# Performance work log

Hardware: AMD Instinct MI355X
Metric: run time of the kernel (lower is better)

Reference implementation:

```python
import jax, jax.numpy as jnp
import numpy as np

B, N, D = 8, 512, 512          # batch, seq_len, n_units (== d_in for residual)
H = 8                          # n_heads
DH = D // H                    # head dim
POS_CLIP = 60
EPS = 1e-7


def setup_inputs() -> dict:
    key = jax.random.key(0)
    ks = jax.random.split(key, 16)
    s = 0.02
    inp = {
        "query": jax.random.normal(ks[0], (B, N, D), dtype=jnp.float32),
        "valid_len": jax.random.randint(ks[1], (B,), 256, N + 1, dtype=jnp.int32),
        "Wq": jax.random.normal(ks[2], (D, D), dtype=jnp.float32) * s,
        "bq": jnp.zeros((D,), jnp.float32),
        "Wk": jax.random.normal(ks[3], (D, D), dtype=jnp.float32) * s,
        "bk": jnp.zeros((D,), jnp.float32),
        "Wv": jax.random.normal(ks[4], (D, D), dtype=jnp.float32) * s,
        "bv": jnp.zeros((D,), jnp.float32),
        "Wh": jax.random.normal(ks[5], (D, D), dtype=jnp.float32) * s,
        "bh": jnp.zeros((D,), jnp.float32),
        "pos_k": jax.random.uniform(ks[6], (2 * POS_CLIP + 1, DH), dtype=jnp.float32, minval=-0.05, maxval=0.05),
        "conv1_w": jax.random.normal(ks[7], (5, 5, H, 2 * H), dtype=jnp.float32) * s,  # HWIO
        "conv1_b": jnp.zeros((2 * H,), jnp.float32),
        "norm1_gamma": jnp.ones((2 * H,), jnp.float32),
        "norm1_beta": jnp.zeros((2 * H,), jnp.float32),
        "conv2_w": jax.random.normal(ks[8], (5, 5, 2 * H, H), dtype=jnp.float32) * s,
        "conv2_b": jnp.zeros((H,), jnp.float32),
        "ln_gamma": jnp.ones((D,), jnp.float32),
        "ln_beta": jnp.zeros((D,), jnp.float32),
    }
    return inp


def _conv_same(x, k, b):
    # x: [b, n, n, cin], k: [kh, kw, cin, cout] -> [b, n, n, cout]
    y = jax.lax.conv_general_dilated(x, k, window_strides=(1, 1), padding="SAME",
                                     dimension_numbers=("NHWC", "HWIO", "NHWC"))
    return y + b


def _norm_masked(x, valid_len, gamma, beta):
    # Norm(axes=[1,2]) with tf.nn.weighted_moments; mask over the query axis (axis 1).
    b, n, m, c = x.shape
    w = (jnp.arange(n)[None, :] < valid_len[:, None]).astype(x.dtype)  # [b, n]
    w4 = w[:, :, None, None]
    sw = valid_len.astype(x.dtype)[:, None, None, None] * m            # sum of broadcast weights
    mean = jnp.sum(w4 * x, axis=(1, 2), keepdims=True) / sw
    var = jnp.sum(w4 * (x - mean) ** 2, axis=(1, 2), keepdims=True) / sw
    return gamma * (x - mean) * jax.lax.rsqrt(var + EPS) + beta


def reference(query, valid_len, Wq, bq, Wk, bk, Wv, bv, Wh, bh, pos_k,
              conv1_w, conv1_b, norm1_gamma, norm1_beta, conv2_w, conv2_b,
              ln_gamma, ln_beta):
    b, n, d_in = query.shape
    # relative position indices (Shaw et al.), clipped to +/- POS_CLIP
    rel = jnp.clip(jnp.arange(n)[None, :] - jnp.arange(n)[:, None], -POS_CLIP, POS_CLIP) + POS_CLIP
    pos_enc = pos_k[rel]                                   # [n, n, dh]

    def heads(x):
        # tf.concat(tf.split(x, H, -1), 0): head-major blocks of size b
        return x.reshape(b, n, H, DH).transpose(2, 0, 1, 3)  # [h, b, n, dh]

    q = heads(query @ Wq + bq)
    k = heads(query @ Wk + bk)
    v = heads(query @ Wv + bv)

    scores = jnp.einsum("hbnd,hbmd->hbnm", q, k) + jnp.einsum("hbnd,nmd->hbnm", q, pos_enc)
    scores = scores / jnp.sqrt(jnp.asarray(DH, scores.dtype))

    # SelfCNN over attention maps: [b, n, n, h]
    maps = scores.transpose(1, 2, 3, 0)
    y = _conv_same(maps, conv1_w, conv1_b)
    y = _norm_masked(y, valid_len, norm1_gamma, norm1_beta)
    y = jax.nn.relu(y)
    y = _conv_same(y, conv2_w, conv2_b)                    # [b, n, n, h]
    scores = y.transpose(3, 0, 1, 2)                       # [h, b, n, m]

    seq_mask = jnp.arange(n)[None, :] < valid_len[:, None]  # [b, n] over key axis
    scores = jnp.where(seq_mask[None, :, None, :], scores, jnp.asarray(-1e12, scores.dtype))
    attn = jax.nn.softmax(scores, axis=-1)

    out = jnp.einsum("hbnm,hbmd->hbnd", attn, v)
    out = out.transpose(1, 2, 0, 3).reshape(b, n, H * DH)  # merge heads back
    out = out @ Wh + bh + query                            # residual

    mean = jnp.mean(out, axis=-1, keepdims=True)
    var = jnp.var(out, axis=-1, keepdims=True)
    return ln_gamma * (out - mean) * jax.lax.rsqrt(var + EPS) + ln_beta
```

## Files before the change

kernel.cpp:

```cpp
#include <hip/hip_runtime.h>

#define PC_ 60

typedef unsigned short u16;
typedef __attribute__((ext_vector_type(8))) short short8v;
typedef __attribute__((ext_vector_type(4))) float f32x4;

__device__ inline float bf2f(u16 u) {
    union { unsigned int i; float f; } x; x.i = ((unsigned)u) << 16; return x.f;
}
__device__ inline u16 f2bf(float f) {
    union { float f; unsigned int i; } x; x.f = f;
    unsigned int r = x.i + 0x7fff + ((x.i >> 16) & 1);
    return (u16)(r >> 16);
}
__device__ inline unsigned pk2(float a, float b) {
    return (unsigned)f2bf(a) | ((unsigned)f2bf(b) << 16);
}

__global__ __launch_bounds__(256) void k_prepx(const float* __restrict__ X, u16* __restrict__ Xb)
{
    const int i = (blockIdx.x * 256 + threadIdx.x) * 8;
    float4 a = *reinterpret_cast<const float4*>(X + i);
    float4 b = *reinterpret_cast<const float4*>(X + i + 4);
    *reinterpret_cast<uint4*>(Xb + i) =
        make_uint4(pk2(a.x, a.y), pk2(a.z, a.w), pk2(b.x, b.y), pk2(b.z, b.w));
}

__global__ __launch_bounds__(256) void k_prept(
    const float* __restrict__ W0, const float* __restrict__ W1,
    const float* __restrict__ W2, const float* __restrict__ W3,
    u16* __restrict__ T0, u16* __restrict__ T1, u16* __restrict__ T2, u16* __restrict__ T3)
{
    const int z = blockIdx.z;
    const float* W = (z == 0) ? W0 : (z == 1) ? W1 : (z == 2) ? W2 : W3;
    u16* T        = (z == 0) ? T0 : (z == 1) ? T1 : (z == 2) ? T2 : T3;
    __shared__ float ls[64 * 65];
    const int k0 = blockIdx.x * 64, n0 = blockIdx.y * 64;
    const int t = threadIdx.x;
#pragma unroll
    for (int i = 0; i < 16; ++i) {
        const int idx = t + i * 256, r = idx >> 6, c = idx & 63;
        ls[c * 65 + r] = W[(size_t)(k0 + r) * 512 + n0 + c];
    }
    __syncthreads();
#pragma unroll
    for (int i = 0; i < 16; ++i) {
        const int idx = t + i * 256, r = idx >> 6, c = idx & 63;
        T[(size_t)(n0 + r) * 512 + k0 + c] = f2bf(ls[r * 65 + c]);
    }
}

__global__ void k_wprep(const float* __restrict__ c1w, const float* __restrict__ c2w,
                        const float* __restrict__ pos_k,
                        u16* __restrict__ Wf1, u16* __restrict__ Wf2, u16* __restrict__ pos_kb)
{
    const int t = threadIdx.x;
    for (int s = t; s < 448; s += 256) {
        const int q = s >> 6, l = s & 63, lg = l >> 4, n = l & 15;
        const int G = q * 4 + lg;
        unsigned o[4];
#pragma unroll
        for (int u2 = 0; u2 < 4; ++u2) {
            float v0 = 0.f, v1 = 0.f;
            if (G < 25) {
                const int dn = G / 5, dm = G - dn * 5;
                v0 = c1w[((dn * 5 + dm) * 8 + u2 * 2 + 0) * 16 + n];
                v1 = c1w[((dn * 5 + dm) * 8 + u2 * 2 + 1) * 16 + n];
            }
            o[u2] = pk2(v0, v1);
        }
        *reinterpret_cast<uint4*>(&Wf1[s * 8]) = make_uint4(o[0], o[1], o[2], o[3]);
    }
    for (int s = t; s < 832; s += 256) {
        const int q = s >> 6, l = s & 63, lg = l >> 4, n = l & 15;
        const int G = q * 4 + lg;
        unsigned o[4];
#pragma unroll
        for (int u2 = 0; u2 < 4; ++u2) {
            float v0 = 0.f, v1 = 0.f;
            if (G < 50 && n < 8) {
                const int pos = G >> 1, h = G & 1;
                const int dn = pos / 5, dm = pos - dn * 5;
                v0 = c2w[((dn * 5 + dm) * 16 + h * 8 + u2 * 2 + 0) * 8 + n];
                v1 = c2w[((dn * 5 + dm) * 16 + h * 8 + u2 * 2 + 1) * 8 + n];
            }
            o[u2] = pk2(v0, v1);
        }
        *reinterpret_cast<uint4*>(&Wf2[s * 8]) = make_uint4(o[0], o[1], o[2], o[3]);
    }
    for (int s = t; s < 128 * 64; s += 256) {
        const int r = s >> 6;
        pos_kb[s] = (r < 121) ? f2bf(pos_k[s]) : (u16)0;
    }
}

__global__ __launch_bounds__(256) void k_qkvm(
    const u16* __restrict__ Xb,
    const u16* __restrict__ WT0, const u16* __restrict__ WT1, const u16* __restrict__ WT2,
    const float* __restrict__ b0, const float* __restrict__ b1, const float* __restrict__ b2,
    u16* __restrict__ Qb, u16* __restrict__ Kb, u16* __restrict__ Vt)
{
    const int z = blockIdx.z;
    const u16* WT    = (z == 0) ? WT0 : (z == 1) ? WT1 : WT2;
    const float* bias = (z == 0) ? b0 : (z == 1) ? b1 : b2;
    __shared__ __align__(16) u16 sh[18432];
    u16* As = sh; u16* Bs = sh + 9216;
    const int t = threadIdx.x, lane = t & 63, wave = t >> 6;
    const int wm = wave >> 1, wn = wave & 1;
    const int lg = lane >> 4, ln16 = lane & 15;
    const int m0 = blockIdx.x * 128, n0 = blockIdx.y * 128;
    f32x4 acc[4][4] = {};
    for (int k0 = 0; k0 < 512; k0 += 64) {
#pragma unroll
        for (int u = 0; u < 4; ++u) {
            const int chunk = u * 256 + t, row = chunk >> 3, ko = (chunk & 7) * 8;
            *reinterpret_cast<uint4*>(As + row * 72 + ko) =
                *reinterpret_cast<const uint4*>(Xb + (size_t)(m0 + row) * 512 + k0 + ko);
            *reinterpret_cast<uint4*>(Bs + row * 72 + ko) =
                *reinterpret_cast<const uint4*>(WT + (size_t)(n0 + row) * 512 + k0 + ko);
        }
        __syncthreads();
#pragma unroll
        for (int kk = 0; kk < 64; kk += 32) {
            short8v a[4], bfr[4];
#pragma unroll
            for (int mi = 0; mi < 4; ++mi)
                a[mi] = *reinterpret_cast<const short8v*>(As + (wm * 64 + mi * 16 + ln16) * 72 + kk + lg * 8);
#pragma unroll
            for (int ni = 0; ni < 4; ++ni)
                bfr[ni] = *reinterpret_cast<const short8v*>(Bs + (wn * 64 + ni * 16 + ln16) * 72 + kk + lg * 8);
#pragma unroll
            for (int mi = 0; mi < 4; ++mi)
#pragma unroll
                for (int ni = 0; ni < 4; ++ni)
                    acc[mi][ni] = __builtin_amdgcn_mfma_f32_16x16x32_bf16(a[mi], bfr[ni], acc[mi][ni], 0, 0, 0);
        }
        __syncthreads();
    }
    u16* Cs = sh + wave * 4608;
#pragma unroll
    for (int ni = 0; ni < 4; ++ni) {
        const float bv = bias[n0 + wn * 64 + ni * 16 + ln16];
#pragma unroll
        for (int mi = 0; mi < 4; ++mi)
#pragma unroll
            for (int r = 0; r < 4; ++r)
                Cs[(mi * 16 + lg * 4 + r) * 72 + ni * 16 + ln16] = f2bf(acc[mi][ni][r] + bv);
    }
    if (z < 2) {
        u16* O = (z == 0) ? Qb : Kb;
#pragma unroll
        for (int j = 0; j < 8; ++j) {
            const int chunk = j * 64 + lane, row = chunk >> 3, co = (chunk & 7) * 8;
            const int tok = m0 + wm * 64 + row;
            const int b = tok >> 9, n = tok & 511;
            const int cg = n0 + wn * 64 + co;
            const int h = cg >> 6, dh = cg & 63;
            *reinterpret_cast<uint4*>(O + ((size_t)((b * 8 + h) * 512 + n)) * 64 + dh) =
                *reinterpret_cast<const uint4*>(Cs + row * 72 + co);
        }
    } else {
#pragma unroll
        for (int j = 0; j < 8; ++j) {
            const int chunk = j * 64 + lane, dr = chunk >> 3, no8 = (chunk & 7) * 8;
            const int cg = n0 + wn * 64 + dr;
            const int h = cg >> 6, dh = cg & 63;
            const int tok = m0 + wm * 64 + no8;
            const int b = tok >> 9, n = tok & 511;
            u16 v[8];
#pragma unroll
            for (int e = 0; e < 8; ++e) v[e] = Cs[(no8 + e) * 72 + dr];
            uint4 o = make_uint4((unsigned)v[0] | ((unsigned)v[1] << 16),
                                 (unsigned)v[2] | ((unsigned)v[3] << 16),
                                 (unsigned)v[4] | ((unsigned)v[5] << 16),
                                 (unsigned)v[6] | ((unsigned)v[7] << 16));
            *reinterpret_cast<uint4*>(Vt + ((size_t)((b * 8 + h) * 64 + dh)) * 512 + n) = o;
        }
    }
}

__global__ __launch_bounds__(256) void k_qposm(
    const u16* __restrict__ Qb, const u16* __restrict__ pos_kb, u16* __restrict__ QP)
{
    __shared__ __align__(16) u16 sh[18432];
    u16* As = sh; u16* Bs = sh + 9216;
    const int t = threadIdx.x, lane = t & 63, wave = t >> 6;
    const int lg = lane >> 4, ln16 = lane & 15;
    const int n0 = blockIdx.x * 128, bh = blockIdx.y;
#pragma unroll
    for (int u = 0; u < 4; ++u) {
        const int chunk = u * 256 + t, row = chunk >> 3, ko = (chunk & 7) * 8;
        *reinterpret_cast<uint4*>(As + row * 72 + ko) =
            *reinterpret_cast<const uint4*>(Qb + ((size_t)(bh * 512 + n0 + row)) * 64 + ko);
        *reinterpret_cast<uint4*>(Bs + row * 72 + ko) =
            *reinterpret_cast<const uint4*>(pos_kb + (size_t)row * 64 + ko);
    }
    __syncthreads();
    f32x4 acc[2][8] = {};
#pragma unroll
    for (int kk = 0; kk < 64; kk += 32) {
        short8v a[2], bfr[8];
#pragma unroll
        for (int mi = 0; mi < 2; ++mi)
            a[mi] = *reinterpret_cast<const short8v*>(As + (wave * 32 + mi * 16 + ln16) * 72 + kk + lg * 8);
#pragma unroll
        for (int ni = 0; ni < 8; ++ni)
            bfr[ni] = *reinterpret_cast<const short8v*>(Bs + (ni * 16 + ln16) * 72 + kk + lg * 8);
#pragma unroll
        for (int mi = 0; mi < 2; ++mi)
#pragma unroll
            for (int ni = 0; ni < 8; ++ni)
                acc[mi][ni] = __builtin_amdgcn_mfma_f32_16x16x32_bf16(a[mi], bfr[ni], acc[mi][ni], 0, 0, 0);
    }
    __syncthreads();
    u16* Cs = sh + wave * 4352;
#pragma unroll
    for (int mi = 0; mi < 2; ++mi)
#pragma unroll
        for (int ni = 0; ni < 8; ++ni)
#pragma unroll
            for (int r = 0; r < 4; ++r)
                Cs[(mi * 16 + lg * 4 + r) * 136 + ni * 16 + ln16] = f2bf(acc[mi][ni][r]);
#pragma unroll
    for (int j = 0; j < 8; ++j) {
        const int chunk = j * 64 + lane, row = chunk >> 4, co = (chunk & 15) * 8;
        *reinterpret_cast<uint4*>(QP + ((size_t)(bh * 512 + n0 + wave * 32 + row)) * 128 + co) =
            *reinterpret_cast<const uint4*>(Cs + row * 136 + co);
    }
}

__global__ __launch_bounds__(256) void k_scoresm(
    const u16* __restrict__ Qb, const u16* __restrict__ Kb, const u16* __restrict__ QP,
    u16* __restrict__ S)
{
    __shared__ __align__(16) u16 sh[18432];
    u16* As = sh; u16* Bs = sh + 9216;
    const int t = threadIdx.x, lane = t & 63, wave = t >> 6;
    const int wm = wave >> 1, wn = wave & 1;
    const int lg = lane >> 4, ln16 = lane & 15;
    const int m0 = blockIdx.x * 128, n0 = blockIdx.y * 128, bh = blockIdx.z;
#pragma unroll
    for (int u = 0; u < 4; ++u) {
        const int chunk = u * 256 + t, row = chunk >> 3, ko = (chunk & 7) * 8;
        *reinterpret_cast<uint4*>(As + row * 72 + ko) =
            *reinterpret_cast<const uint4*>(Qb + ((size_t)(bh * 512 + n0 + row)) * 64 + ko);
        *reinterpret_cast<uint4*>(Bs + row * 72 + ko) =
            *reinterpret_cast<const uint4*>(Kb + ((size_t)(bh * 512 + m0 + row)) * 64 + ko);
    }
    __syncthreads();
    f32x4 acc[4][4] = {};
#pragma unroll
    for (int kk = 0; kk < 64; kk += 32) {
        short8v a[4], bfr[4];
#pragma unroll
        for (int mi = 0; mi < 4; ++mi)
            a[mi] = *reinterpret_cast<const short8v*>(As + (wm * 64 + mi * 16 + ln16) * 72 + kk + lg * 8);
#pragma unroll
        for (int ni = 0; ni < 4; ++ni)
            bfr[ni] = *reinterpret_cast<const short8v*>(Bs + (wn * 64 + ni * 16 + ln16) * 72 + kk + lg * 8);
#pragma unroll
        for (int mi = 0; mi < 4; ++mi)
#pragma unroll
            for (int ni = 0; ni < 4; ++ni)
                acc[mi][ni] = __builtin_amdgcn_mfma_f32_16x16x32_bf16(a[mi], bfr[ni], acc[mi][ni], 0, 0, 0);
    }
    __syncthreads();
    u16* QPs = sh;
#pragma unroll
    for (int u = 0; u < 8; ++u) {
        const int chunk = u * 256 + t, row = chunk >> 4, co = (chunk & 15) * 8;
        *reinterpret_cast<uint4*>(QPs + row * 128 + co) =
            *reinterpret_cast<const uint4*>(QP + ((size_t)(bh * 512 + n0 + row)) * 128 + co);
    }
    __syncthreads();
#pragma unroll
    for (int mi = 0; mi < 4; ++mi)
#pragma unroll
        for (int ni = 0; ni < 4; ++ni) {
            const int m_g = m0 + wn * 64 + ni * 16 + ln16;
#pragma unroll
            for (int r = 0; r < 4; ++r) {
                const int n_loc = wm * 64 + mi * 16 + lg * 4 + r;
                const int n_g = n0 + n_loc;
                int rel = m_g - n_g;
                rel = rel < -PC_ ? -PC_ : (rel > PC_ ? PC_ : rel);
                const float v = (acc[mi][ni][r] + bf2f(QPs[n_loc * 128 + rel + PC_])) * 0.125f;
                S[(size_t)bh * 262144 + (size_t)n_g * 512 + m_g] = f2bf(v);
            }
        }
}

__global__ __launch_bounds__(256) void k_conv1m(
    const u16* __restrict__ S, const u16* __restrict__ Wf,
    const float* __restrict__ bias, u16* __restrict__ Y,
    const int* __restrict__ VL, float* __restrict__ ST)
{
    __shared__ __align__(16) u16 xs[10368];
    __shared__ float wred[4][16][2];
    const int t = threadIdx.x;
    const int b = blockIdx.z;
    const int n0 = blockIdx.y * 32;
    const int m0 = blockIdx.x * 32;
    const u16* sp0 = S + (size_t)(b * 8) * 262144;
    for (int idx = t; idx < 1296; idx += 256) {
        const int r = idx / 36; const int c = idx - r * 36;
        const int gn = n0 - 2 + r, gm = m0 - 2 + c;
        uint4 pk = make_uint4(0, 0, 0, 0);
        if ((unsigned)gn < 512u && (unsigned)gm < 512u) {
            const u16* p = sp0 + (size_t)gn * 512 + gm;
            u16 v[8];
#pragma unroll
            for (int e = 0; e < 8; ++e) v[e] = p[(size_t)e * 262144];
            pk.x = (unsigned)v[0] | ((unsigned)v[1] << 16);
            pk.y = (unsigned)v[2] | ((unsigned)v[3] << 16);
            pk.z = (unsigned)v[4] | ((unsigned)v[5] << 16);
            pk.w = (unsigned)v[6] | ((unsigned)v[7] << 16);
        }
        *reinterpret_cast<uint4*>(&xs[idx * 8]) = pk;
    }
    const int lane = t & 63, wave = t >> 6;
    const int lg = lane >> 4, ln16 = lane & 15;
    short8v bq[7];
#pragma unroll
    for (int q = 0; q < 7; ++q)
        bq[q] = *reinterpret_cast<const short8v*>(&Wf[(q * 64 + lane) * 8]);
    int aoff[7];
#pragma unroll
    for (int q = 0; q < 7; ++q) {
        const int G = q * 4 + lg; const int p = (G < 25) ? G : 0;
        const int dn = p / 5, dm = p - dn * 5;
        aoff[q] = (dn * 36 + dm) * 8;
    }
    const float bs = bias[ln16];
    const int vl = VL[b];
    float sst = 0.f, sst2 = 0.f;
    __syncthreads();
    for (int i = 0; i < 16; ++i) {
        const int j = wave * 16 + i;
        const int tr = j >> 1, c0 = (j & 1) << 4;
        const int pb = (tr * 36 + c0 + ln16) * 8;
        f32x4 acc = {bs, bs, bs, bs};
#pragma unroll
        for (int q = 0; q < 7; ++q) {
            short8v a = *reinterpret_cast<const short8v*>(&xs[pb + aoff[q]]);
            acc = __builtin_amdgcn_mfma_f32_16x16x32_bf16(a, bq[q], acc, 0, 0, 0);
        }
        u16* yp = Y + (((size_t)(b * 512 + n0 + tr)) * 512 + (m0 + c0 + lg * 4)) * 16 + ln16;
        yp[0]  = f2bf(acc[0]); yp[16] = f2bf(acc[1]);
        yp[32] = f2bf(acc[2]); yp[48] = f2bf(acc[3]);
        if (n0 + tr < vl) {
            sst  += acc[0] + acc[1] + acc[2] + acc[3];
            sst2 += acc[0]*acc[0] + acc[1]*acc[1] + acc[2]*acc[2] + acc[3]*acc[3];
        }
    }
    sst  += __shfl_xor(sst, 16);  sst  += __shfl_xor(sst, 32);
    sst2 += __shfl_xor(sst2, 16); sst2 += __shfl_xor(sst2, 32);
    if (lane < 16) { wred[wave][lane][0] = sst; wred[wave][lane][1] = sst2; }
    __syncthreads();
    if (t < 16) {
        const float a  = wred[0][t][0] + wred[1][t][0] + wred[2][t][0] + wred[3][t][0];
        const float b2 = wred[0][t][1] + wred[1][t][1] + wred[2][t][1] + wred[3][t][1];
        atomicAdd(&ST[(b * 16 + t) * 2 + 0], a);
        atomicAdd(&ST[(b * 16 + t) * 2 + 1], b2);
    }
}

__global__ void k_statfin(const float* __restrict__ ST, const int* __restrict__ VL,
                          const float* __restrict__ g, const float* __restrict__ be,
                          float* __restrict__ ST2)
{
    const int i = threadIdx.x;
    if (i < 128) {
        const int b = i >> 4, c = i & 15;
        const float sw = (float)VL[b] * 512.f;
        const float mean = ST[i * 2] / sw;
        const float var = ST[i * 2 + 1] / sw - mean * mean;
        const float scale = g[c] * rsqrtf(var + 1e-7f);
        ST2[i * 2] = scale;
        ST2[i * 2 + 1] = be[c] - mean * scale;
    }
}

__global__ __launch_bounds__(256) void k_conv2m(
    const u16* __restrict__ Y, const float* __restrict__ ST2,
    const u16* __restrict__ Wf, const float* __restrict__ bias,
    u16* __restrict__ S2)
{
    __shared__ __align__(16) u16 xs[20736];
    const int t = threadIdx.x;
    const int b = blockIdx.z;
    const int n0 = blockIdx.y * 32, m0 = blockIdx.x * 32;
    float sc[16], shv[16];
#pragma unroll
    for (int ch = 0; ch < 16; ++ch) {
        sc[ch]  = ST2[(b * 16 + ch) * 2 + 0];
        shv[ch] = ST2[(b * 16 + ch) * 2 + 1];
    }
    for (int idx = t; idx < 1296; idx += 256) {
        const int r = idx / 36; const int c = idx - r * 36;
        const int gn = n0 - 2 + r, gm = m0 - 2 + c;
        uint4 p0 = make_uint4(0, 0, 0, 0), p1 = p0;
        if ((unsigned)gn < 512u && (unsigned)gm < 512u) {
            const u16* yp = Y + (((size_t)(b * 512 + gn)) * 512 + gm) * 16;
            const uint4 r0 = *reinterpret_cast<const uint4*>(yp);
            const uint4 r1 = *reinterpret_cast<const uint4*>(yp + 8);
            const unsigned w0[4] = {r0.x, r0.y, r0.z, r0.w};
            const unsigned w1[4] = {r1.x, r1.y, r1.z, r1.w};
            unsigned o0[4], o1[4];
#pragma unroll
            for (int u2 = 0; u2 < 4; ++u2) {
                const int ch = u2 * 2;
                float a0 = bf2f((u16)(w0[u2] & 0xffff));
                float a1 = bf2f((u16)(w0[u2] >> 16));
                a0 = fmaf(a0, sc[ch], shv[ch]);          a0 = a0 > 0.f ? a0 : 0.f;
                a1 = fmaf(a1, sc[ch + 1], shv[ch + 1]);  a1 = a1 > 0.f ? a1 : 0.f;
                o0[u2] = pk2(a0, a1);
                const int ch2 = 8 + u2 * 2;
                float b0 = bf2f((u16)(w1[u2] & 0xffff));
                float b1 = bf2f((u16)(w1[u2] >> 16));
                b0 = fmaf(b0, sc[ch2], shv[ch2]);          b0 = b0 > 0.f ? b0 : 0.f;
                b1 = fmaf(b1, sc[ch2 + 1], shv[ch2 + 1]);  b1 = b1 > 0.f ? b1 : 0.f;
                o1[u2] = pk2(b0, b1);
            }
            p0 = make_uint4(o0[0], o0[1], o0[2], o0[3]);
            p1 = make_uint4(o1[0], o1[1], o1[2], o1[3]);
        }
        *reinterpret_cast<uint4*>(&xs[idx * 8]) = p0;
        *reinterpret_cast<uint4*>(&xs[10368 + idx * 8]) = p1;
    }
    const int lane = t & 63, wave = t >> 6;
    const int lg = lane >> 4, ln16 = lane & 15;
    short8v bq[13];
#pragma unroll
    for (int q = 0; q < 13; ++q)
        bq[q] = *reinterpret_cast<const short8v*>(&Wf[(q * 64 + lane) * 8]);
    int aoff[13];
#pragma unroll
    for (int q = 0; q < 13; ++q) {
        const int G = q * 4 + lg; const int p = (G < 50) ? G : 0;
        const int pos = p >> 1, h = p & 1;
        const int dn = pos / 5, dm = pos - dn * 5;
        aoff[q] = h * 10368 + (dn * 36 + dm) * 8;
    }
    const float bs = (ln16 < 8) ? bias[ln16] : 0.f;
    __syncthreads();
    for (int i = 0; i < 16; ++i) {
        const int j = wave * 16 + i;
        const int tr = j >> 1, c0 = (j & 1) << 4;
        const int pb = (tr * 36 + c0 + ln16) * 8;
        f32x4 acc = {bs, bs, bs, bs};
#pragma unroll
        for (int q = 0; q < 13; ++q) {
            short8v a = *reinterpret_cast<const short8v*>(&xs[pb + aoff[q]]);
            acc = __builtin_amdgcn_mfma_f32_16x16x32_bf16(a, bq[q], acc, 0, 0, 0);
        }
        if (ln16 < 8) {
            uint2 o = make_uint2(pk2(acc[0], acc[1]), pk2(acc[2], acc[3]));
            *reinterpret_cast<uint2*>(
                &S2[(((size_t)(b * 8 + ln16)) * 512 + n0 + tr) * 512 + m0 + c0 + lg * 4]) = o;
        }
    }
}

__global__ __launch_bounds__(256) void k_softmax(u16* __restrict__ S,
                                                 const int* __restrict__ VL)
{
    const int row = blockIdx.x * 4 + (threadIdx.x >> 6);
    const int lane = threadIdx.x & 63;
    const int b = row >> 12;
    const int vl = VL[b];
    u16* p = S + (size_t)row * 512;
    uint4 v = *reinterpret_cast<const uint4*>(p + lane * 8);
    const unsigned w[4] = {v.x, v.y, v.z, v.w};
    float vals[8];
#pragma unroll
    for (int j = 0; j < 4; ++j) {
        vals[2 * j]     = bf2f((u16)(w[j] & 0xffff));
        vals[2 * j + 1] = bf2f((u16)(w[j] >> 16));
    }
    const int mbase = lane * 8;
    float mx = -3.0e38f;
#pragma unroll
    for (int j = 0; j < 8; ++j) {
        if (mbase + j >= vl) vals[j] = -3.0e38f;
        mx = fmaxf(mx, vals[j]);
    }
#pragma unroll
    for (int o = 32; o; o >>= 1) mx = fmaxf(mx, __shfl_xor(mx, o));
    float sum = 0.f;
#pragma unroll
    for (int j = 0; j < 8; ++j) {
        const float e = __expf(vals[j] - mx);
        vals[j] = e;
        sum += e;
    }
#pragma unroll
    for (int o = 32; o; o >>= 1) sum += __shfl_xor(sum, o);
    const float inv = 1.0f / sum;
    uint4 ov = make_uint4(pk2(vals[0] * inv, vals[1] * inv), pk2(vals[2] * inv, vals[3] * inv),
                          pk2(vals[4] * inv, vals[5] * inv), pk2(vals[6] * inv, vals[7] * inv));
    *reinterpret_cast<uint4*>(p + lane * 8) = ov;
}

__global__ __launch_bounds__(256) void k_avm(
    const u16* __restrict__ P, const u16* __restrict__ Vt, u16* __restrict__ X2)
{
    __shared__ __align__(16) u16 sh[13824];
    u16* As = sh; u16* Bs = sh + 9216;
    const int t = threadIdx.x, lane = t & 63, wave = t >> 6;
    const int lg = lane >> 4, ln16 = lane & 15;
    const int n0 = blockIdx.x * 128, bh = blockIdx.y;
    const int b = bh >> 3, h = bh & 7;
    f32x4 acc[2][4] = {};
    for (int k0 = 0; k0 < 512; k0 += 64) {
#pragma unroll
        for (int u = 0; u < 4; ++u) {
            const int chunk = u * 256 + t, row = chunk >> 3, ko = (chunk & 7) * 8;
            *reinterpret_cast<uint4*>(As + row * 72 + ko) =
                *reinterpret_cast<const uint4*>(P + ((size_t)(bh * 512 + n0 + row)) * 512 + k0 + ko);
        }
#pragma unroll
        for (int u = 0; u < 2; ++u) {
            const int chunk = u * 256 + t, row = chunk >> 3, ko = (chunk & 7) * 8;
            *reinterpret_cast<uint4*>(Bs + row * 72 + ko) =
                *reinterpret_cast<const uint4*>(Vt + ((size_t)(bh * 64 + row)) * 512 + k0 + ko);
        }
        __syncthreads();
#pragma unroll
        for (int kk = 0; kk < 64; kk += 32) {
            short8v a[2], bfr[4];
#pragma unroll
            for (int mi = 0; mi < 2; ++mi)
                a[mi] = *reinterpret_cast<const short8v*>(As + (wave * 32 + mi * 16 + ln16) * 72 + kk + lg * 8);
#pragma unroll
            for (int ni = 0; ni < 4; ++ni)
                bfr[ni] = *reinterpret_cast<const short8v*>(Bs + (ni * 16 + ln16) * 72 + kk + lg * 8);
#pragma unroll
            for (int mi = 0; mi < 2; ++mi)
#pragma unroll
                for (int ni = 0; ni < 4; ++ni)
                    acc[mi][ni] = __builtin_amdgcn_mfma_f32_16x16x32_bf16(a[mi], bfr[ni], acc[mi][ni], 0, 0, 0);
        }
        __syncthreads();
    }
    u16* Cs = sh + wave * 2304;
#pragma unroll
    for (int mi = 0; mi < 2; ++mi)
#pragma unroll
        for (int ni = 0; ni < 4; ++ni)
#pragma unroll
            for (int r = 0; r < 4; ++r)
                Cs[(mi * 16 + lg * 4 + r) * 72 + ni * 16 + ln16] = f2bf(acc[mi][ni][r]);
#pragma unroll
    for (int j = 0; j < 4; ++j) {
        const int chunk = j * 64 + lane, row = chunk >> 3, co = (chunk & 7) * 8;
        const int tn = n0 + wave * 32 + row;
        *reinterpret_cast<uint4*>(X2 + ((size_t)(b * 512 + tn)) * 512 + h * 64 + co) =
            *reinterpret_cast<const uint4*>(Cs + row * 72 + co);
    }
}

__global__ __launch_bounds__(256) void k_outm(
    const u16* __restrict__ X2, const u16* __restrict__ WT, const float* __restrict__ bias,
    const float* __restrict__ Xq, float* __restrict__ Pout)
{
    __shared__ __align__(16) u16 sh[18432];
    u16* As = sh; u16* Bs = sh + 9216;
    const int t = threadIdx.x, lane = t & 63, wave = t >> 6;
    const int wm = wave >> 1, wn = wave & 1;
    const int lg = lane >> 4, ln16 = lane & 15;
    const int m0 = blockIdx.x * 128, n0 = blockIdx.y * 128;
    f32x4 acc[4][4] = {};
    for (int k0 = 0; k0 < 512; k0 += 64) {
#pragma unroll
        for (int u = 0; u < 4; ++u) {
            const int chunk = u * 256 + t, row = chunk >> 3, ko = (chunk & 7) * 8;
            *reinterpret_cast<uint4*>(As + row * 72 + ko) =
                *reinterpret_cast<const uint4*>(X2 + (size_t)(m0 + row) * 512 + k0 + ko);
            *reinterpret_cast<uint4*>(Bs + row * 72 + ko) =
                *reinterpret_cast<const uint4*>(WT + (size_t)(n0 + row) * 512 + k0 + ko);
        }
        __syncthreads();
#pragma unroll
        for (int kk = 0; kk < 64; kk += 32) {
            short8v a[4], bfr[4];
#pragma unroll
            for (int mi = 0; mi < 4; ++mi)
                a[mi] = *reinterpret_cast<const short8v*>(As + (wm * 64 + mi * 16 + ln16) * 72 + kk + lg * 8);
#pragma unroll
            for (int ni = 0; ni < 4; ++ni)
                bfr[ni] = *reinterpret_cast<const short8v*>(Bs + (wn * 64 + ni * 16 + ln16) * 72 + kk + lg * 8);
#pragma unroll
            for (int mi = 0; mi < 4; ++mi)
#pragma unroll
                for (int ni = 0; ni < 4; ++ni)
                    acc[mi][ni] = __builtin_amdgcn_mfma_f32_16x16x32_bf16(a[mi], bfr[ni], acc[mi][ni], 0, 0, 0);
        }
        __syncthreads();
    }
#pragma unroll
    for (int ni = 0; ni < 4; ++ni) {
        const int cg = n0 + wn * 64 + ni * 16 + ln16;
        const float bv = bias[cg];
#pragma unroll
        for (int mi = 0; mi < 4; ++mi)
#pragma unroll
            for (int r = 0; r < 4; ++r) {
                const int tok = m0 + wm * 64 + mi * 16 + lg * 4 + r;
                Pout[(size_t)tok * 512 + cg] = acc[mi][ni][r] + bv + Xq[(size_t)tok * 512 + cg];
            }
    }
}

__global__ __launch_bounds__(256) void k_ln(
    const float* __restrict__ P, const float* __restrict__ g,
    const float* __restrict__ be, float* __restrict__ out)
{
    const int row = blockIdx.x * 4 + (threadIdx.x >> 6);
    const int lane = threadIdx.x & 63;
    const float* p = P + (size_t)row * 512;
    float4 v0 = reinterpret_cast<const float4*>(p)[lane];
    float4 v1 = reinterpret_cast<const float4*>(p)[64 + lane];
    float s = v0.x + v0.y + v0.z + v0.w + v1.x + v1.y + v1.z + v1.w;
#pragma unroll
    for (int o = 32; o; o >>= 1) s += __shfl_xor(s, o);
    const float mean = s * (1.0f / 512.0f);
    float d[8] = {v0.x - mean, v0.y - mean, v0.z - mean, v0.w - mean,
                  v1.x - mean, v1.y - mean, v1.z - mean, v1.w - mean};
    float s2 = 0.f;
#pragma unroll
    for (int j = 0; j < 8; ++j) s2 += d[j] * d[j];
#pragma unroll
    for (int o = 32; o; o >>= 1) s2 += __shfl_xor(s2, o);
    const float rstd = rsqrtf(s2 * (1.0f / 512.0f) + 1e-7f);
    float4 g0 = reinterpret_cast<const float4*>(g)[lane];
    float4 g1 = reinterpret_cast<const float4*>(g)[64 + lane];
    float4 b0 = reinterpret_cast<const float4*>(be)[lane];
    float4 b1 = reinterpret_cast<const float4*>(be)[64 + lane];
    float* op = out + (size_t)row * 512;
    reinterpret_cast<float4*>(op)[lane] =
        make_float4(d[0] * rstd * g0.x + b0.x, d[1] * rstd * g0.y + b0.y,
                    d[2] * rstd * g0.z + b0.z, d[3] * rstd * g0.w + b0.w);
    reinterpret_cast<float4*>(op)[64 + lane] =
        make_float4(d[4] * rstd * g1.x + b1.x, d[5] * rstd * g1.y + b1.y,
                    d[6] * rstd * g1.z + b1.z, d[7] * rstd * g1.w + b1.w);
}

extern "C" void kernel_launch(void* const* d_in, const int* in_sizes, int n_in,
                              void* d_out, int out_size, void* d_ws, size_t ws_size,
                              hipStream_t stream)
{
    const float* query = (const float*)d_in[0];
    const int*   VL    = (const int*)d_in[1];
    const float* Wq = (const float*)d_in[2];  const float* bq = (const float*)d_in[3];
    const float* Wk = (const float*)d_in[4];  const float* bk = (const float*)d_in[5];
    const float* Wv = (const float*)d_in[6];  const float* bv = (const float*)d_in[7];
    const float* Wh = (const float*)d_in[8];  const float* bh = (const float*)d_in[9];
    const float* pos_k = (const float*)d_in[10];
    const float* c1w = (const float*)d_in[11]; const float* c1b = (const float*)d_in[12];
    const float* n1g = (const float*)d_in[13]; const float* n1b = (const float*)d_in[14];
    const float* c2w = (const float*)d_in[15]; const float* c2b = (const float*)d_in[16];
    const float* lng = (const float*)d_in[17]; const float* lnb = (const float*)d_in[18];

    float* ws = (float*)d_ws;
    const size_t M1 = (size_t)1 << 20;
    u16* S1  = (u16*)ws;
    u16* Y1  = (u16*)(ws + 8 * M1);
    u16* Xb  = (u16*)(ws + 24 * M1);
    u16* Qb  = (u16*)(ws + 25 * M1);
    u16* Kb  = (u16*)(ws + 26 * M1);
    u16* Vt  = (u16*)(ws + 27 * M1);
    u16* QPb = (u16*)(ws + 28 * M1);
    u16* WqT = (u16*)(ws + 30 * M1);
    u16* WkT = WqT + 262144;
    u16* WvT = WkT + 262144;
    u16* WhT = WvT + 262144;
    u16* pos_kb = (u16*)(ws + 30 * M1 + 524288);
    u16* Wf1 = pos_kb + 8192;
    u16* Wf2 = Wf1 + 3584;
    float* ST  = ws + 31 * M1;
    float* ST2 = ST + 256;
    u16* X2 = Xb;
    float* Pout = ws + 28 * M1;

    hipMemsetAsync(ST, 0, 256 * sizeof(float), stream);

    k_prepx<<<1024, 256, 0, stream>>>(query, Xb);
    k_prept<<<dim3(8, 8, 4), 256, 0, stream>>>(Wq, Wk, Wv, Wh, WqT, WkT, WvT, WhT);
    k_wprep<<<1, 256, 0, stream>>>(c1w, c2w, pos_k, Wf1, Wf2, pos_kb);
    k_qkvm<<<dim3(32, 4, 3), 256, 0, stream>>>(Xb, WqT, WkT, WvT, bq, bk, bv, Qb, Kb, Vt);
    k_qposm<<<dim3(4, 64), 256, 0, stream>>>(Qb, pos_kb, QPb);
    k_scoresm<<<dim3(4, 4, 64), 256, 0, stream>>>(Qb, Kb, QPb, S1);
    k_conv1m<<<dim3(16, 16, 8), 256, 0, stream>>>(S1, Wf1, c1b, Y1, VL, ST);
    k_statfin<<<1, 128, 0, stream>>>(ST, VL, n1g, n1b, ST2);
    k_conv2m<<<dim3(16, 16, 8), 256, 0, stream>>>(Y1, ST2, Wf2, c2b, S1);
    k_softmax<<<8192, 256, 0, stream>>>(S1, VL);
    k_avm<<<dim3(4, 64), 256, 0, stream>>>(S1, Vt, X2);
    k_outm<<<dim3(32, 4), 256, 0, stream>>>(X2, WhT, bh, query, Pout);
    k_ln<<<1024, 256, 0, stream>>>(Pout, lng, lnb, (float*)d_out);
}
```

Baseline: 286.5 us.

## Fuse softmax into AV matmul, merge prep kernels, inline norm stats

Merges the query cast, weight transposes and conv/pos weight prep into one launch. Folds the norm-statistics finalize into conv2, and fuses softmax into the attention-times-V matmul: row max and sum are computed first, then exp is applied while staging A tiles. This removes the separate softmax read and write of the score tensor and cuts the kernel launch count. Conv1 output stores are also widened by pairing adjacent channels through lane shuffles. The cost is that k_softav reads the scores twice, has a serial per-row stats phase in only 256 blocks, and recomputes exp during staging.

Measured after the change: 312.0 us. 8.9% more time.

```diff
diff --git a/kernel.cpp b/kernel.cpp
--- a/kernel.cpp
+++ b/kernel.cpp
@@ -18,26 +18,74 @@
     return (unsigned)f2bf(a) | ((unsigned)f2bf(b) << 16);
 }
 
-__global__ __launch_bounds__(256) void k_prepx(const float* __restrict__ X, u16* __restrict__ Xb)
-{
-    const int i = (blockIdx.x * 256 + threadIdx.x) * 8;
-    float4 a = *reinterpret_cast<const float4*>(X + i);
-    float4 b = *reinterpret_cast<const float4*>(X + i + 4);
-    *reinterpret_cast<uint4*>(Xb + i) =
-        make_uint4(pk2(a.x, a.y), pk2(a.z, a.w), pk2(b.x, b.y), pk2(b.z, b.w));
-}
-
 __global__ __launch_bounds__(256) void k_prept(
     const float* __restrict__ W0, const float* __restrict__ W1,
     const float* __restrict__ W2, const float* __restrict__ W3,
-    u16* __restrict__ T0, u16* __restrict__ T1, u16* __restrict__ T2, u16* __restrict__ T3)
+    u16* __restrict__ T0, u16* __restrict__ T1, u16* __restrict__ T2, u16* __restrict__ T3,
+    const float* __restrict__ c1w, const float* __restrict__ c2w,
+    const float* __restrict__ pos_k,
+    u16* __restrict__ Wf1, u16* __restrict__ Wf2, u16* __restrict__ pos_kb,
+    const float* __restrict__ X, u16* __restrict__ Xb)
 {
     const int z = blockIdx.z;
+    const int t = threadIdx.x;
+    if (z == 5) {
+        const int blk = blockIdx.y * 8 + blockIdx.x;
+#pragma unroll
+        for (int k2 = 0; k2 < 16; ++k2) {
+            const int i = ((blk * 16 + k2) * 256 + t) * 8;
+            float4 a = *reinterpret_cast<const float4*>(X + i);
+            float4 b = *reinterpret_cast<const float4*>(X + i + 4);
+            *reinterpret_cast<uint4*>(Xb + i) =
+                make_uint4(pk2(a.x, a.y), pk2(a.z, a.w), pk2(b.x, b.y), pk2(b.z, b.w));
+        }
+        return;
+    }
+    if (z == 4) {
+        if (blockIdx.x != 0 || blockIdx.y != 0) return;
+        for (int s = t; s < 448; s += 256) {
+            const int q = s >> 6, l = s & 63, lg = l >> 4, n = l & 15;
+            const int G = q * 4 + lg;
+            unsigned o[4];
+#pragma unroll
+            for (int u2 = 0; u2 < 4; ++u2) {
+                float v0 = 0.f, v1 = 0.f;
+                if (G < 25) {
+                    const int dn = G / 5, dm = G - dn * 5;
+                    v0 = c1w[((dn * 5 + dm) * 8 + u2 * 2 + 0) * 16 + n];
+                    v1 = c1w[((dn * 5 + dm) * 8 + u2 * 2 + 1) * 16 + n];
+                }
+                o[u2] = pk2(v0, v1);
+            }
+            *reinterpret_cast<uint4*>(&Wf1[s * 8]) = make_uint4(o[0], o[1], o[2], o[3]);
+        }
+        for (int s = t; s < 832; s += 256) {
+            const int q = s >> 6, l = s & 63, lg = l >> 4, n = l & 15;
+            const int G = q * 4 + lg;
+            unsigned o[4];
+#pragma unroll
+            for (int u2 = 0; u2 < 4; ++u2) {
+                float v0 = 0.f, v1 = 0.f;
+                if (G < 50 && n < 8) {
+                    const int pos = G >> 1, h = G & 1;
+                    const int dn = pos / 5, dm = pos - dn * 5;
+                    v0 = c2w[((dn * 5 + dm) * 16 + h * 8 + u2 * 2 + 0) * 8 + n];
+                    v1 = c2w[((dn * 5 + dm) * 16 + h * 8 + u2 * 2 + 1) * 8 + n];
+                }
+                o[u2] = pk2(v0, v1);
+            }
+            *reinterpret_cast<uint4*>(&Wf2[s * 8]) = make_uint4(o[0], o[1], o[2], o[3]);
+        }
+        for (int s = t; s < 128 * 64; s += 256) {
+            const int r = s >> 6;
+            pos_kb[s] = (r < 121) ? f2bf(pos_k[s]) : (u16)0;
+        }
+        return;
+    }
     const float* W = (z == 0) ? W0 : (z == 1) ? W1 : (z == 2) ? W2 : W3;
     u16* T        = (z == 0) ? T0 : (z == 1) ? T1 : (z == 2) ? T2 : T3;
     __shared__ float ls[64 * 65];
     const int k0 = blockIdx.x * 64, n0 = blockIdx.y * 64;
-    const int t = threadIdx.x;
 #pragma unroll
     for (int i = 0; i < 16; ++i) {
         const int idx = t + i * 256, r = idx >> 6, c = idx & 63;
@@ -48,50 +96,6 @@
     for (int i = 0; i < 16; ++i) {
         const int idx = t + i * 256, r = idx >> 6, c = idx & 63;
         T[(size_t)(n0 + r) * 512 + k0 + c] = f2bf(ls[r * 65 + c]);
-    }
-}
-
-__global__ void k_wprep(const float* __restrict__ c1w, const float* __restrict__ c2w,
-                        const float* __restrict__ pos_k,
-                        u16* __restrict__ Wf1, u16* __restrict__ Wf2, u16* __restrict__ pos_kb)
-{
-    const int t = threadIdx.x;
-    for (int s = t; s < 448; s += 256) {
-        const int q = s >> 6, l = s & 63, lg = l >> 4, n = l & 15;
-        const int G = q * 4 + lg;
-        unsigned o[4];
-#pragma unroll
-        for (int u2 = 0; u2 < 4; ++u2) {
-            float v0 = 0.f, v1 = 0.f;
-            if (G < 25) {
-                const int dn = G / 5, dm = G - dn * 5;
-                v0 = c1w[((dn * 5 + dm) * 8 + u2 * 2 + 0) * 16 + n];
-                v1 = c1w[((dn * 5 + dm) * 8 + u2 * 2 + 1) * 16 + n];
-            }
-            o[u2] = pk2(v0, v1);
-        }
-        *reinterpret_cast<uint4*>(&Wf1[s * 8]) = make_uint4(o[0], o[1], o[2], o[3]);
-    }
-    for (int s = t; s < 832; s += 256) {
-        const int q = s >> 6, l = s & 63, lg = l >> 4, n = l & 15;
-        const int G = q * 4 + lg;
-        unsigned o[4];
-#pragma unroll
-        for (int u2 = 0; u2 < 4; ++u2) {
-            float v0 = 0.f, v1 = 0.f;
-            if (G < 50 && n < 8) {
-                const int pos = G >> 1, h = G & 1;
-                const int dn = pos / 5, dm = pos - dn * 5;
-                v0 = c2w[((dn * 5 + dm) * 16 + h * 8 + u2 * 2 + 0) * 8 + n];
-                v1 = c2w[((dn * 5 + dm) * 16 + h * 8 + u2 * 2 + 1) * 8 + n];
-            }
-            o[u2] = pk2(v0, v1);
-        }
-        *reinterpret_cast<uint4*>(&Wf2[s * 8]) = make_uint4(o[0], o[1], o[2], o[3]);
-    }
-    for (int s = t; s < 128 * 64; s += 256) {
-        const int r = s >> 6;
-        pos_kb[s] = (r < 121) ? f2bf(pos_k[s]) : (u16)0;
     }
 }
 
@@ -334,6 +338,8 @@
     }
     const float bs = bias[ln16];
     const int vl = VL[b];
+    const int cb = ln16 & ~1;
+    const bool evn = (ln16 & 1) == 0;
     float sst = 0.f, sst2 = 0.f;
     __syncthreads();
     for (int i = 0; i < 16; ++i) {
@@ -346,9 +352,20 @@
             short8v a = *reinterpret_cast<const short8v*>(&xs[pb + aoff[q]]);
             acc = __builtin_amdgcn_mfma_f32_16x16x32_bf16(a, bq[q], acc, 0, 0, 0);
         }
-        u16* yp = Y + (((size_t)(b * 512 + n0 + tr)) * 512 + (m0 + c0 + lg * 4)) * 16 + ln16;
-        yp[0]  = f2bf(acc[0]); yp[16] = f2bf(acc[1]);
-        yp[32] = f2bf(acc[2]); yp[48] = f2bf(acc[3]);
+        unsigned wv_[4];
+#pragma unroll
+        for (int r = 0; r < 4; ++r) {
+            const float ex = __shfl_xor(acc[r], 1);
+            wv_[r] = evn ? pk2(acc[r], ex) : pk2(ex, acc[r]);
+        }
+        u16* yb = Y + (((size_t)(b * 512 + n0 + tr)) * 512 + (m0 + c0 + lg * 4)) * 16 + cb;
+        if (evn) {
+            *reinterpret_cast<unsigned*>(yb)      = wv_[0];
+            *reinterpret_cast<unsigned*>(yb + 16) = wv_[1];
+        } else {
+            *reinterpret_cast<unsigned*>(yb + 32) = wv_[2];
+            *reinterpret_cast<unsigned*>(yb + 48) = wv_[3];
+        }
         if (n0 + tr < vl) {
             sst  += acc[0] + acc[1] + acc[2] + acc[3];
             sst2 += acc[0]*acc[0] + acc[1]*acc[1] + acc[2]*acc[2] + acc[3]*acc[3];
@@ -366,37 +383,29 @@
     }
 }
 
-__global__ void k_statfin(const float* __restrict__ ST, const int* __restrict__ VL,
-                          const float* __restrict__ g, const float* __restrict__ be,
-                          float* __restrict__ ST2)
-{
-    const int i = threadIdx.x;
-    if (i < 128) {
-        const int b = i >> 4, c = i & 15;
-        const float sw = (float)VL[b] * 512.f;
-        const float mean = ST[i * 2] / sw;
-        const float var = ST[i * 2 + 1] / sw - mean * mean;
-        const float scale = g[c] * rsqrtf(var + 1e-7f);
-        ST2[i * 2] = scale;
-        ST2[i * 2 + 1] = be[c] - mean * scale;
-    }
-}
-
 __global__ __launch_bounds__(256) void k_conv2m(
-    const u16* __restrict__ Y, const float* __restrict__ ST2,
+    const u16* __restrict__ Y, const float* __restrict__ ST,
+    const int* __restrict__ VL, const float* __restrict__ n1g, const float* __restrict__ n1b,
     const u16* __restrict__ Wf, const float* __restrict__ bias,
     u16* __restrict__ S2)
 {
     __shared__ __align__(16) u16 xs[20736];
+    __shared__ float ssh[16][2];
     const int t = threadIdx.x;
     const int b = blockIdx.z;
     const int n0 = blockIdx.y * 32, m0 = blockIdx.x * 32;
+    if (t < 16) {
+        const float sw = (float)VL[b] * 512.f;
+        const float mean = ST[(b * 16 + t) * 2 + 0] / sw;
+        const float var  = ST[(b * 16 + t) * 2 + 1] / sw - mean * mean;
+        const float sc = n1g[t] * rsqrtf(var + 1e-7f);
+        ssh[t][0] = sc;
+        ssh[t][1] = n1b[t] - mean * sc;
+    }
+    __syncthreads();
     float sc[16], shv[16];
 #pragma unroll
-    for (int ch = 0; ch < 16; ++ch) {
-        sc[ch]  = ST2[(b * 16 + ch) * 2 + 0];
-        shv[ch] = ST2[(b * 16 + ch) * 2 + 1];
-    }
+    for (int ch = 0; ch < 16; ++ch) { sc[ch] = ssh[ch][0]; shv[ch] = ssh[ch][1]; }
     for (int idx = t; idx < 1296; idx += 256) {
         const int r = idx / 36; const int c = idx - r * 36;
         const int gn = n0 - 2 + r, gm = m0 - 2 + c;
@@ -463,62 +472,63 @@
     }
 }
 
-__global__ __launch_bounds__(256) void k_softmax(u16* __restrict__ S,
-                                                 const int* __restrict__ VL)
-{
-    const int row = blockIdx.x * 4 + (threadIdx.x >> 6);
-    const int lane = threadIdx.x & 63;
-    const int b = row >> 12;
-    const int vl = VL[b];
-    u16* p = S + (size_t)row * 512;
-    uint4 v = *reinterpret_cast<const uint4*>(p + lane * 8);
-    const unsigned w[4] = {v.x, v.y, v.z, v.w};
-    float vals[8];
-#pragma unroll
-    for (int j = 0; j < 4; ++j) {
-        vals[2 * j]     = bf2f((u16)(w[j] & 0xffff));
-        vals[2 * j + 1] = bf2f((u16)(w[j] >> 16));
-    }
-    const int mbase = lane * 8;
-    float mx = -3.0e38f;
-#pragma unroll
-    for (int j = 0; j < 8; ++j) {
-        if (mbase + j >= vl) vals[j] = -3.0e38f;
-        mx = fmaxf(mx, vals[j]);
-    }
-#pragma unroll
-    for (int o = 32; o; o >>= 1) mx = fmaxf(mx, __shfl_xor(mx, o));
-    float sum = 0.f;
-#pragma unroll
-    for (int j = 0; j < 8; ++j) {
-        const float e = __expf(vals[j] - mx);
-        vals[j] = e;
-        sum += e;
-    }
-#pragma unroll
-    for (int o = 32; o; o >>= 1) sum += __shfl_xor(sum, o);
-    const float inv = 1.0f / sum;
-    uint4 ov = make_uint4(pk2(vals[0] * inv, vals[1] * inv), pk2(vals[2] * inv, vals[3] * inv),
-                          pk2(vals[4] * inv, vals[5] * inv), pk2(vals[6] * inv, vals[7] * inv));
-    *reinterpret_cast<uint4*>(p + lane * 8) = ov;
-}
-
-__global__ __launch_bounds__(256) void k_avm(
-    const u16* __restrict__ P, const u16* __restrict__ Vt, u16* __restrict__ X2)
-{
-    __shared__ __align__(16) u16 sh[13824];
-    u16* As = sh; u16* Bs = sh + 9216;
+__global__ __launch_bounds__(256) void k_softav(
+    const u16* __restrict__ SL, const u16* __restrict__ Vt,
+    const int* __restrict__ VL, u16* __restrict__ X2)
+{
+    __shared__ __align__(16) u16 As[9216];
+    __shared__ __align__(16) u16 Bs[4608];
+    __shared__ float smx[128], siv[128];
     const int t = threadIdx.x, lane = t & 63, wave = t >> 6;
     const int lg = lane >> 4, ln16 = lane & 15;
     const int n0 = blockIdx.x * 128, bh = blockIdx.y;
     const int b = bh >> 3, h = bh & 7;
+    const int vl = VL[b];
+    const u16* Sp = SL + (size_t)bh * 262144;
+    for (int rr = 0; rr < 32; ++rr) {
+        const int row = wave * 32 + rr;
+        uint4 v = *reinterpret_cast<const uint4*>(Sp + (size_t)(n0 + row) * 512 + lane * 8);
+        const unsigned w[4] = {v.x, v.y, v.z, v.w};
+        float x[8];
+#pragma unroll
+        for (int j = 0; j < 4; ++j) {
+            x[2 * j]     = bf2f((u16)(w[j] & 0xffff));
+            x[2 * j + 1] = bf2f((u16)(w[j] >> 16));
+        }
+        const int mb = lane * 8;
+        float mx = -3.0e38f;
+#pragma unroll
+        for (int j = 0; j < 8; ++j) {
+            if (mb + j >= vl) x[j] = -3.0e38f;
+            mx = fmaxf(mx, x[j]);
+        }
+#pragma unroll
+        for (int o = 32; o; o >>= 1) mx = fmaxf(mx, __shfl_xor(mx, o));
+        float sm = 0.f;
+#pragma unroll
+        for (int j = 0; j < 8; ++j) sm += __expf(x[j] - mx);
+#pragma unroll
+        for (int o = 32; o; o >>= 1) sm += __shfl_xor(sm, o);
+        if (lane == 0) { smx[row] = mx; siv[row] = 1.0f / sm; }
+    }
+    __syncthreads();
     f32x4 acc[2][4] = {};
     for (int k0 = 0; k0 < 512; k0 += 64) {
 #pragma unroll
         for (int u = 0; u < 4; ++u) {
             const int chunk = u * 256 + t, row = chunk >> 3, ko = (chunk & 7) * 8;
-            *reinterpret_cast<uint4*>(As + row * 72 + ko) =
-                *reinterpret_cast<const uint4*>(P + ((size_t)(bh * 512 + n0 + row)) * 512 + k0 + ko);
+            uint4 raw = *reinterpret_cast<const uint4*>(Sp + (size_t)(n0 + row) * 512 + k0 + ko);
+            const unsigned w[4] = {raw.x, raw.y, raw.z, raw.w};
+            const float mxr = smx[row], ivr = siv[row];
+            unsigned o[4];
+#pragma unroll
+            for (int jj = 0; jj < 4; ++jj) {
+                const int m0i = k0 + ko + 2 * jj;
+                float a0 = (m0i     < vl) ? __expf(bf2f((u16)(w[jj] & 0xffff)) - mxr) * ivr : 0.f;
+                float a1 = (m0i + 1 < vl) ? __expf(bf2f((u16)(w[jj] >> 16))   - mxr) * ivr : 0.f;
+                o[jj] = pk2(a0, a1);
+            }
+            *reinterpret_cast<uint4*>(As + row * 72 + ko) = make_uint4(o[0], o[1], o[2], o[3]);
         }
 #pragma unroll
         for (int u = 0; u < 2; ++u) {
@@ -544,7 +554,7 @@
         }
         __syncthreads();
     }
-    u16* Cs = sh + wave * 2304;
+    u16* Cs = As + wave * 2304;
 #pragma unroll
     for (int mi = 0; mi < 2; ++mi)
 #pragma unroll
@@ -680,23 +690,20 @@
     u16* Wf1 = pos_kb + 8192;
     u16* Wf2 = Wf1 + 3584;
     float* ST  = ws + 31 * M1;
-    float* ST2 = ST + 256;
     u16* X2 = Xb;
     float* Pout = ws + 28 * M1;
 
     hipMemsetAsync(ST, 0, 256 * sizeof(float), stream);
 
-    k_prepx<<<1024, 256, 0, stream>>>(query, Xb);
-    k_prept<<<dim3(8, 8, 4), 256, 0, stream>>>(Wq, Wk, Wv, Wh, WqT, WkT, WvT, WhT);
-    k_wprep<<<1, 256, 0, stream>>>(c1w, c2w, pos_k, Wf1, Wf2, pos_kb);
+    k_prept<<<dim3(8, 8, 6), 256, 0, stream>>>(Wq, Wk, Wv, Wh, WqT, WkT, WvT, WhT,
+                                               c1w, c2w, pos_k, Wf1, Wf2, pos_kb,
+                                               query, Xb);
     k_qkvm<<<dim3(32, 4, 3), 256, 0, stream>>>(Xb, WqT, WkT, WvT, bq, bk, bv, Qb, Kb, Vt);
     k_qposm<<<dim3(4, 64), 256, 0, stream>>>(Qb, pos_kb, QPb);
     k_scoresm<<<dim3(4, 4, 64), 256, 0, stream>>>(Qb, Kb, QPb, S1);
     k_conv1m<<<dim3(16, 16, 8), 256, 0, stream>>>(S1, Wf1, c1b, Y1, VL, ST);
-    k_statfin<<<1, 128, 0, stream>>>(ST, VL, n1g, n1b, ST2);
-    k_conv2m<<<dim3(16, 16, 8), 256, 0, stream>>>(Y1, ST2, Wf2, c2b, S1);
-    k_softmax<<<8192, 256, 0, stream>>>(S1, VL);
-    k_avm<<<dim3(4, 64), 256, 0, stream>>>(S1, Vt, X2);
+    k_conv2m<<<dim3(16, 16, 8), 256, 0, stream>>>(Y1, ST, VL, n1g, n1b, Wf2, c2b, S1);
+    k_softav<<<dim3(4, 64), 256, 0, stream>>>(S1, Vt, VL, X2);
     k_outm<<<dim3(32, 4), 256, 0, stream>>>(X2, WhT, bh, query, Pout);
     k_ln<<<1024, 256, 0, stream>>>(Pout, lng, lnb, (float*)d_out);
 }
```
